# Performance work log

Measured on AMD Instinct MI355X. Metric: run time of the kernel, lower is better.

Reference implementation:

```python
import jax, jax.numpy as jnp
import numpy as np
from jax import lax

N_IN = 512
N_OUT = 512
T = 2048
N_OBS = 256


def setup_inputs() -> dict:
    key = jax.random.key(0)
    k1, k2, k3, k4 = jax.random.split(key, 4)
    X = jax.random.normal(k1, (T, N_IN), dtype=jnp.float32)
    # W_init ~ randn / sqrt(n_input), matching the module's default init scale
    W_init = jax.random.normal(k2, (N_OUT, N_IN), dtype=jnp.float32) / np.sqrt(N_IN)
    theta = jax.random.normal(k3, (2,), dtype=jnp.float32) * 0.1
    observed_idx = jnp.sort(jax.random.randint(k4, (N_OBS,), 0, N_OUT, dtype=jnp.int32))
    return {"X": X, "W_init": W_init, "theta": theta, "observed_idx": observed_idx}


def reference(X, W_init, theta, observed_idx):
    lr = 1.0 / X.shape[1]  # module default lr = 1/n_input

    def step(W, x):
        y = jax.nn.sigmoid(W @ x)                       # [n_out]
        # parametrized Oja/Hebbian plasticity rule:
        #   dW = theta0 * y x^T + theta1 * y^2 * W
        dW = theta[0] * jnp.outer(y, x) + theta[1] * (y * y)[:, None] * W
        W_next = W + lr * dW
        m = y[observed_idx]                             # observed subset
        return W_next, m

    _, m_traj = lax.scan(step, W_init, X)               # m_traj: [T, n_obs]
    return m_traj
```

## Files before the change

### kernel.cpp

```cpp
#include <hip/hip_runtime.h>


constexpr int N_IN    = 512;
constexpr int T       = 2048;
constexpr int N_OBS   = 256;
constexpr int D       = 8;
constexpr int NBLK    = T / D;
constexpr int BANDPAD = 64;
constexpr float LOG2E = 1.44269504088896f;

typedef float f4 __attribute__((ext_vector_type(4)));

__device__ constexpr int BOFF[8] = {0, 7, 13, 18, 22, 25, 27, 28};

#define DPP_ADD(v, ctrl, rmask)                                                \
    v += __int_as_float(__builtin_amdgcn_update_dpp(                           \
        0, __float_as_int(v), (ctrl), (rmask), 0xf, false))

__device__ __forceinline__ float wave64_sum_bcast(float v) {
    DPP_ADD(v, 0x111, 0xf);
    DPP_ADD(v, 0x112, 0xf);
    DPP_ADD(v, 0x114, 0xf);
    DPP_ADD(v, 0x118, 0xf);
    DPP_ADD(v, 0x142, 0xa);
    DPP_ADD(v, 0x143, 0xc);
    return __int_as_float(__builtin_amdgcn_readlane(__float_as_int(v), 63));
}

__device__ __forceinline__ float dot8s(const f4& w0, const f4& w1,
                                       const f4& x0, const f4& x1) {
    float p = w0.x * x0.x;
    p = fmaf(w0.y, x0.y, p);
    p = fmaf(w0.z, x0.z, p);
    p = fmaf(w0.w, x0.w, p);
    p = fmaf(w1.x, x1.x, p);
    p = fmaf(w1.y, x1.y, p);
    p = fmaf(w1.z, x1.z, p);
    p = fmaf(w1.w, x1.w, p);
    return p;
}

#define GLOADX(dst, addr, offstr)                                              \
    asm volatile("global_load_dwordx4 %0, %1, off offset:" offstr              \
                 : "=v"(dst) : "v"(addr))

__device__ __forceinline__ void stage16(f4 (&xb)[16], const char* xa) {
    const char* a0 = xa;
    const char* a1 = xa + 4096;
    const char* a2 = xa + 8192;
    const char* a3 = xa + 12288;
    GLOADX(xb[0],  a0, "0");    GLOADX(xb[1],  a0, "1024");
    GLOADX(xb[2],  a0, "2048"); GLOADX(xb[3],  a0, "3072");
    GLOADX(xb[4],  a1, "0");    GLOADX(xb[5],  a1, "1024");
    GLOADX(xb[6],  a1, "2048"); GLOADX(xb[7],  a1, "3072");
    GLOADX(xb[8],  a2, "0");    GLOADX(xb[9],  a2, "1024");
    GLOADX(xb[10], a2, "2048"); GLOADX(xb[11], a2, "3072");
    GLOADX(xb[12], a3, "0");    GLOADX(xb[13], a3, "1024");
    GLOADX(xb[14], a3, "2048"); GLOADX(xb[15], a3, "3072");
}

#define TIEBUF(ins, buf)                                                       \
    asm volatile(ins                                                           \
        : "+v"(buf[0]), "+v"(buf[1]), "+v"(buf[2]),  "+v"(buf[3]),             \
          "+v"(buf[4]), "+v"(buf[5]), "+v"(buf[6]),  "+v"(buf[7]),             \
          "+v"(buf[8]), "+v"(buf[9]), "+v"(buf[10]), "+v"(buf[11]),            \
          "+v"(buf[12]),"+v"(buf[13]),"+v"(buf[14]), "+v"(buf[15]))

#define PIN(buf)      TIEBUF("", buf)
#define WAIT1(buf)    TIEBUF("s_waitcnt vmcnt(1)", buf)
#define WAIT0(buf)    TIEBUF("s_waitcnt vmcnt(0)", buf)

__global__ __launch_bounds__(64) void gram_kernel(const float* __restrict__ X,
                                                  float* __restrict__ P) {
    const int b    = blockIdx.x;
    const int lane = threadIdx.x;
    const int t0   = b * D;
    const f4* Xv = (const f4*)(X + (long)t0 * N_IN);
    f4 r[8][2];
    #pragma unroll
    for (int i = 0; i < 8; ++i) {
        r[i][0] = Xv[i * (N_IN / 4) + lane * 2 + 0];
        r[i][1] = Xv[i * (N_IN / 4) + lane * 2 + 1];
    }
    float s[28];
    #pragma unroll
    for (int i = 0; i < 7; ++i) {
        #pragma unroll
        for (int j = 1; j <= 7 - i; ++j) {
            s[BOFF[i] + j - 1] =
                wave64_sum_bcast(dot8s(r[i][0], r[i][1], r[i + j][0], r[i + j][1]));
        }
    }
    if (lane == 0) {
        #pragma unroll
        for (int k = 0; k < 28; ++k) P[b * BANDPAD + k] = s[k];
    }
}

__device__ __forceinline__ void process_block(
    const f4 (&xb)[16], const float (&bs)[28], int t0, int lane, int wave,
    f4& w0, f4& w1, float th0s, float th1, float* __restrict__ out)
{
    float q[D];
    #pragma unroll
    for (int d = 0; d < D; ++d)
        q[d] = wave64_sum_bcast(dot8s(w0, w1, xb[2 * d], xb[2 * d + 1]));

    float av[D], bv[D];
    float ys = 0.0f;
    float z = q[0];
    #pragma unroll
    for (int i = 0; i < D; ++i) {
        const float y =
            __builtin_amdgcn_rcpf(1.0f + __builtin_amdgcn_exp2f(-z));
        if (lane == i) ys = y;

        const float a = th0s * y;
        const float b = fmaf(th1 * y, y, 1.0f);
        av[i] = a;
        bv[i] = b;

        #pragma unroll
        for (int d = i + 1; d < D; ++d)
            q[d] = fmaf(b, q[d], a * bs[BOFF[i] + (d - i) - 1]);
        if (i < D - 1) z = q[i + 1];
    }

    float c[D];
    float sfx = 1.0f;
    #pragma unroll
    for (int i = D - 1; i >= 0; --i) {
        c[i] = av[i] * sfx;
        sfx *= bv[i];
    }
    const float B = sfx;

    f4 acc0, acc1;
    acc0.x = c[0] * xb[0].x;  acc0.y = c[0] * xb[0].y;
    acc0.z = c[0] * xb[0].z;  acc0.w = c[0] * xb[0].w;
    acc1.x = c[0] * xb[1].x;  acc1.y = c[0] * xb[1].y;
    acc1.z = c[0] * xb[1].z;  acc1.w = c[0] * xb[1].w;
    #pragma unroll
    for (int i = 1; i < D; ++i) {
        acc0.x = fmaf(c[i], xb[2 * i].x, acc0.x);
        acc0.y = fmaf(c[i], xb[2 * i].y, acc0.y);
        acc0.z = fmaf(c[i], xb[2 * i].z, acc0.z);
        acc0.w = fmaf(c[i], xb[2 * i].w, acc0.w);
        acc1.x = fmaf(c[i], xb[2 * i + 1].x, acc1.x);
        acc1.y = fmaf(c[i], xb[2 * i + 1].y, acc1.y);
        acc1.z = fmaf(c[i], xb[2 * i + 1].z, acc1.z);
        acc1.w = fmaf(c[i], xb[2 * i + 1].w, acc1.w);
    }
    w0.x = fmaf(B, w0.x, acc0.x);
    w0.y = fmaf(B, w0.y, acc0.y);
    w0.z = fmaf(B, w0.z, acc0.z);
    w0.w = fmaf(B, w0.w, acc0.w);
    w1.x = fmaf(B, w1.x, acc1.x);
    w1.y = fmaf(B, w1.y, acc1.y);
    w1.z = fmaf(B, w1.z, acc1.z);
    w1.w = fmaf(B, w1.w, acc1.w);

    float* oaddr = out + (size_t)(t0 + lane) * N_OBS + wave;
    asm volatile("s_mov_b64 vcc, exec\n\t"
                 "s_mov_b64 exec, 0xff\n\t"
                 "global_store_dword %0, %1, off\n\t"
                 "s_mov_b64 exec, vcc"
                 :: "v"(oaddr), "v"(ys) : "vcc");
}

__device__ __forceinline__ void load_band(float (&bs)[28], const float* pb) {
    #pragma unroll
    for (int k = 0; k < 28; ++k) bs[k] = pb[k];
}

__global__ __launch_bounds__(256, 1) void oja_scan_kernel(
    const float* __restrict__ X,
    const float* __restrict__ Winit,
    const float* __restrict__ theta,
    const int*   __restrict__ obs,
    const float* __restrict__ P,
    float*       __restrict__ out)
{
    const int tid  = threadIdx.x;
    const int wid  = tid >> 6;
    const int lane = tid & 63;
    const int wave = blockIdx.x * 4 + wid;

    const int row = obs[wave];
    const float lr   = 1.0f / (float)N_IN;
    const float th0s = theta[0] * lr * LOG2E;
    const float th1  = theta[1] * lr;

    const f4* Wv = (const f4*)(Winit + (long)row * N_IN);
    f4 w0 = Wv[lane];
    f4 w1 = Wv[64 + lane];
    w0.x *= LOG2E; w0.y *= LOG2E; w0.z *= LOG2E; w0.w *= LOG2E;
    w1.x *= LOG2E; w1.y *= LOG2E; w1.z *= LOG2E; w1.w *= LOG2E;

    const char* xbase = (const char*)X + (size_t)lane * 16;

    f4 xA[16], xB[16];
    float bsA[28], bsB[28];

    stage16(xA, xbase);
    load_band(bsA, P);
    WAIT0(xA);

    for (int blk = 0; blk < NBLK; blk += 2) {
        const int b1 = (blk + 1 < NBLK) ? (blk + 1) : (NBLK - 1);
        stage16(xB, xbase + (size_t)b1 * 16384);
        load_band(bsB, P + (size_t)b1 * BANDPAD);
        PIN(xA);
        process_block(xA, bsA, blk * D, lane, wave, w0, w1, th0s, th1, out);
        WAIT1(xB);

        const int b2 = (blk + 2 < NBLK) ? (blk + 2) : (NBLK - 1);
        stage16(xA, xbase + (size_t)b2 * 16384);
        load_band(bsA, P + (size_t)b2 * BANDPAD);
        PIN(xB);
        process_block(xB, bsB, (blk + 1) * D, lane, wave, w0, w1, th0s, th1, out);
        WAIT1(xA);
    }
}

extern "C" void kernel_launch(void* const* d_in, const int* in_sizes, int n_in,
                              void* d_out, int out_size, void* d_ws, size_t ws_size,
                              hipStream_t stream) {
    const float* X     = (const float*)d_in[0];
    const float* Winit = (const float*)d_in[1];
    const float* theta = (const float*)d_in[2];
    const int*   obs   = (const int*)d_in[3];
    float*       out   = (float*)d_out;
    float*       P     = (float*)d_ws;

    gram_kernel<<<NBLK, 64, 0, stream>>>(X, P);

    oja_scan_kernel<<<64, 256, 0, stream>>>(X, Winit, theta, obs, P, out);
}
```

Measured before the change: 248.1 us.

## Split each observed row across four waves with LDS partial-dot reduction

Each observed output row was handled by one wave holding 8 weights per lane. It is now split across a 256-thread block: four waves each own a 128-column slice with 2 weights per lane. Partial dot products are combined through shared memory with one barrier per 8-step block, and the grid grows from 64 to 256 blocks to fill more CUs. This cuts per-wave ALU and load work on the serial critical path, but adds an LDS round trip and a workgroup barrier on every block, and every wave redundantly runs the scalar recurrence.

```diff
diff --git a/kernel.cpp b/kernel.cpp
--- a/kernel.cpp
+++ b/kernel.cpp
@@ -10,6 +10,7 @@
 constexpr float LOG2E = 1.44269504088896f;
 
 typedef float f4 __attribute__((ext_vector_type(4)));
+typedef float f2 __attribute__((ext_vector_type(2)));
 
 __device__ constexpr int BOFF[8] = {0, 7, 13, 18, 22, 25, 27, 28};
 
@@ -40,35 +41,29 @@
     return p;
 }
 
-#define GLOADX(dst, addr, offstr)                                              \
-    asm volatile("global_load_dwordx4 %0, %1, off offset:" offstr              \
+#define GLOADX2(dst, addr, offstr)                                             \
+    asm volatile("global_load_dwordx2 %0, %1, off offset:" offstr              \
                  : "=v"(dst) : "v"(addr))
 
-__device__ __forceinline__ void stage16(f4 (&xb)[16], const char* xa) {
+__device__ __forceinline__ void stage8(f2 (&xb)[8], const char* xa) {
     const char* a0 = xa;
     const char* a1 = xa + 4096;
     const char* a2 = xa + 8192;
     const char* a3 = xa + 12288;
-    GLOADX(xb[0],  a0, "0");    GLOADX(xb[1],  a0, "1024");
-    GLOADX(xb[2],  a0, "2048"); GLOADX(xb[3],  a0, "3072");
-    GLOADX(xb[4],  a1, "0");    GLOADX(xb[5],  a1, "1024");
-    GLOADX(xb[6],  a1, "2048"); GLOADX(xb[7],  a1, "3072");
-    GLOADX(xb[8],  a2, "0");    GLOADX(xb[9],  a2, "1024");
-    GLOADX(xb[10], a2, "2048"); GLOADX(xb[11], a2, "3072");
-    GLOADX(xb[12], a3, "0");    GLOADX(xb[13], a3, "1024");
-    GLOADX(xb[14], a3, "2048"); GLOADX(xb[15], a3, "3072");
-}
-
-#define TIEBUF(ins, buf)                                                       \
+    GLOADX2(xb[0], a0, "0");  GLOADX2(xb[1], a0, "2048");
+    GLOADX2(xb[2], a1, "0");  GLOADX2(xb[3], a1, "2048");
+    GLOADX2(xb[4], a2, "0");  GLOADX2(xb[5], a2, "2048");
+    GLOADX2(xb[6], a3, "0");  GLOADX2(xb[7], a3, "2048");
+}
+
+#define TIEBUF8(ins, buf)                                                      \
     asm volatile(ins                                                           \
-        : "+v"(buf[0]), "+v"(buf[1]), "+v"(buf[2]),  "+v"(buf[3]),             \
-          "+v"(buf[4]), "+v"(buf[5]), "+v"(buf[6]),  "+v"(buf[7]),             \
-          "+v"(buf[8]), "+v"(buf[9]), "+v"(buf[10]), "+v"(buf[11]),            \
-          "+v"(buf[12]),"+v"(buf[13]),"+v"(buf[14]), "+v"(buf[15]))
-
-#define PIN(buf)      TIEBUF("", buf)
-#define WAIT1(buf)    TIEBUF("s_waitcnt vmcnt(1)", buf)
-#define WAIT0(buf)    TIEBUF("s_waitcnt vmcnt(0)", buf)
+        : "+v"(buf[0]), "+v"(buf[1]), "+v"(buf[2]), "+v"(buf[3]),              \
+          "+v"(buf[4]), "+v"(buf[5]), "+v"(buf[6]), "+v"(buf[7]))
+
+#define PIN(buf)      TIEBUF8("", buf)
+#define WAIT1(buf)    TIEBUF8("s_waitcnt vmcnt(1)", buf)
+#define WAIT0(buf)    TIEBUF8("s_waitcnt vmcnt(0)", buf)
 
 __global__ __launch_bounds__(64) void gram_kernel(const float* __restrict__ X,
                                                   float* __restrict__ P) {
@@ -98,13 +93,32 @@
 }
 
 __device__ __forceinline__ void process_block(
-    const f4 (&xb)[16], const float (&bs)[28], int t0, int lane, int wave,
-    f4& w0, f4& w1, float th0s, float th1, float* __restrict__ out)
+    const f2 (&xb)[8], const float (&bs)[28], int t0, int lane, int wid,
+    int col, int buf, float* __restrict__ smem,
+    f2& w, float th0s, float th1, float* __restrict__ out)
 {
+    float qp[D];
+    #pragma unroll
+    for (int d = 0; d < D; ++d) {
+        float p = w.x * xb[d].x;
+        p = fmaf(w.y, xb[d].y, p);
+        qp[d] = wave64_sum_bcast(p);
+    }
+
+    float packv = qp[0];
+    #pragma unroll
+    for (int d = 1; d < D; ++d) packv = (lane == d) ? qp[d] : packv;
+    if (lane < D) smem[buf * 32 + lane * 4 + wid] = packv;
+    asm volatile("s_waitcnt lgkmcnt(0)" ::: "memory");
+    __builtin_amdgcn_s_barrier();
+    asm volatile("" ::: "memory");
+    const f4 qq = *reinterpret_cast<const f4*>(&smem[buf * 32 + (lane & 7) * 4]);
+    const float qsum = (qq.x + qq.y) + (qq.z + qq.w);
     float q[D];
     #pragma unroll
     for (int d = 0; d < D; ++d)
-        q[d] = wave64_sum_bcast(dot8s(w0, w1, xb[2 * d], xb[2 * d + 1]));
+        q[d] = __int_as_float(
+            __builtin_amdgcn_readlane(__float_as_int(qsum), d));
 
     float av[D], bv[D];
     float ys = 0.0f;
@@ -135,32 +149,18 @@
     }
     const float B = sfx;
 
-    f4 acc0, acc1;
-    acc0.x = c[0] * xb[0].x;  acc0.y = c[0] * xb[0].y;
-    acc0.z = c[0] * xb[0].z;  acc0.w = c[0] * xb[0].w;
-    acc1.x = c[0] * xb[1].x;  acc1.y = c[0] * xb[1].y;
-    acc1.z = c[0] * xb[1].z;  acc1.w = c[0] * xb[1].w;
+    f2 acc;
+    acc.x = c[0] * xb[0].x;
+    acc.y = c[0] * xb[0].y;
     #pragma unroll
     for (int i = 1; i < D; ++i) {
-        acc0.x = fmaf(c[i], xb[2 * i].x, acc0.x);
-        acc0.y = fmaf(c[i], xb[2 * i].y, acc0.y);
-        acc0.z = fmaf(c[i], xb[2 * i].z, acc0.z);
-        acc0.w = fmaf(c[i], xb[2 * i].w, acc0.w);
-        acc1.x = fmaf(c[i], xb[2 * i + 1].x, acc1.x);
-        acc1.y = fmaf(c[i], xb[2 * i + 1].y, acc1.y);
-        acc1.z = fmaf(c[i], xb[2 * i + 1].z, acc1.z);
-        acc1.w = fmaf(c[i], xb[2 * i + 1].w, acc1.w);
-    }
-    w0.x = fmaf(B, w0.x, acc0.x);
-    w0.y = fmaf(B, w0.y, acc0.y);
-    w0.z = fmaf(B, w0.z, acc0.z);
-    w0.w = fmaf(B, w0.w, acc0.w);
-    w1.x = fmaf(B, w1.x, acc1.x);
-    w1.y = fmaf(B, w1.y, acc1.y);
-    w1.z = fmaf(B, w1.z, acc1.z);
-    w1.w = fmaf(B, w1.w, acc1.w);
-
-    float* oaddr = out + (size_t)(t0 + lane) * N_OBS + wave;
+        acc.x = fmaf(c[i], xb[i].x, acc.x);
+        acc.y = fmaf(c[i], xb[i].y, acc.y);
+    }
+    w.x = fmaf(B, w.x, acc.x);
+    w.y = fmaf(B, w.y, acc.y);
+
+    float* oaddr = out + (size_t)(t0 + lane) * N_OBS + col;
     asm volatile("s_mov_b64 vcc, exec\n\t"
                  "s_mov_b64 exec, 0xff\n\t"
                  "global_store_dword %0, %1, off\n\t"
@@ -181,44 +181,47 @@
     const float* __restrict__ P,
     float*       __restrict__ out)
 {
+    __shared__ __align__(16) float smem[64];
+
     const int tid  = threadIdx.x;
     const int wid  = tid >> 6;
     const int lane = tid & 63;
-    const int wave = blockIdx.x * 4 + wid;
-
-    const int row = obs[wave];
+    const int col  = blockIdx.x;
+
+    const int row = obs[col];
     const float lr   = 1.0f / (float)N_IN;
     const float th0s = theta[0] * lr * LOG2E;
     const float th1  = theta[1] * lr;
 
-    const f4* Wv = (const f4*)(Winit + (long)row * N_IN);
-    f4 w0 = Wv[lane];
-    f4 w1 = Wv[64 + lane];
-    w0.x *= LOG2E; w0.y *= LOG2E; w0.z *= LOG2E; w0.w *= LOG2E;
-    w1.x *= LOG2E; w1.y *= LOG2E; w1.z *= LOG2E; w1.w *= LOG2E;
-
-    const char* xbase = (const char*)X + (size_t)lane * 16;
-
-    f4 xA[16], xB[16];
+    const f2* Wv = (const f2*)(Winit + (long)row * N_IN + wid * 128);
+    f2 w = Wv[lane];
+    w.x *= LOG2E; w.y *= LOG2E;
+
+    const char* xbase =
+        (const char*)X + (size_t)(wid * 128 + lane * 2) * 4;
+
+    f2 xA[8], xB[8];
     float bsA[28], bsB[28];
 
-    stage16(xA, xbase);
+    stage8(xA, xbase);
     load_band(bsA, P);
     WAIT0(xA);
 
     for (int blk = 0; blk < NBLK; blk += 2) {
         const int b1 = (blk + 1 < NBLK) ? (blk + 1) : (NBLK - 1);
-        stage16(xB, xbase + (size_t)b1 * 16384);
+        stage8(xB, xbase + (size_t)b1 * 16384);
         load_band(bsB, P + (size_t)b1 * BANDPAD);
         PIN(xA);
-        process_block(xA, bsA, blk * D, lane, wave, w0, w1, th0s, th1, out);
+        process_block(xA, bsA, blk * D, lane, wid, col, 0, smem,
+                      w, th0s, th1, out);
         WAIT1(xB);
 
         const int b2 = (blk + 2 < NBLK) ? (blk + 2) : (NBLK - 1);
-        stage16(xA, xbase + (size_t)b2 * 16384);
+        stage8(xA, xbase + (size_t)b2 * 16384);
         load_band(bsA, P + (size_t)b2 * BANDPAD);
         PIN(xB);
-        process_block(xB, bsB, (blk + 1) * D, lane, wave, w0, w1, th0s, th1, out);
+        process_block(xB, bsB, (blk + 1) * D, lane, wid, col, 1, smem,
+                      w, th0s, th1, out);
         WAIT1(xA);
     }
 }
@@ -235,5 +238,5 @@
 
     gram_kernel<<<NBLK, 64, 0, stream>>>(X, P);
 
-    oja_scan_kernel<<<64, 256, 0, stream>>>(X, Winit, theta, obs, P, out);
-}
+    oja_scan_kernel<<<256, 256, 0, stream>>>(X, Winit, theta, obs, P, out);
+}
```

Measured after the change: 315.3 us. +27.1%, slower.
